# Optimization experiments

Measured on AMD Instinct MI355X. Metric: run time of the kernel, lower is better.

## Reference

```python
import jax, jax.numpy as jnp
import numpy as np


def _jpeg_tables():
    y_table = np.array([
        [16, 11, 10, 16, 24, 40, 51, 61],
        [12, 12, 14, 19, 26, 58, 60, 55],
        [14, 13, 16, 24, 40, 57, 69, 56],
        [14, 17, 22, 29, 51, 87, 80, 62],
        [18, 22, 37, 56, 68, 109, 103, 77],
        [24, 35, 55, 64, 81, 104, 113, 92],
        [49, 64, 78, 87, 103, 121, 120, 101],
        [72, 92, 95, 98, 112, 100, 103, 99]], dtype=np.float32)
    c_table = np.full((8, 8), 99.0, dtype=np.float32)
    c_table[:4, :4] = np.array([
        [17, 18, 24, 47],
        [18, 21, 26, 66],
        [24, 26, 56, 99],
        [47, 66, 99, 99]], dtype=np.float32).T
    return y_table, c_table


def _idct_basis():
    # alpha outer product and 8x8x8x8 cosine basis, matching _DeDCT8x8
    a = np.array([1.0 / np.sqrt(2)] + [1.0] * 7)
    alpha = np.outer(a, a).astype(np.float32)
    x = np.arange(8)
    cu = np.cos((2 * x[None, :] + 1) * x[:, None] * np.pi / 16)  # [freq, pos] -> careful
    # tensor[x, y, u, v] = cos((2u+1)x pi/16) * cos((2v+1)y pi/16)
    c = np.cos((2 * x[None, :] + 1) * x[:, None] * np.pi / 16)  # c[f, p]
    tensor = (c[:, None, :, None] * c[None, :, None, :]).astype(np.float32)
    return alpha, tensor


def setup_inputs() -> dict:
    key = jax.random.key(0)
    k1, k2, k3 = jax.random.split(key, 3)
    B, H, W = 8, 2048, 2048
    y = jax.random.normal(k1, (B, (H // 8) * (W // 8), 8, 8), dtype=jnp.float32)
    cb = jax.random.normal(k2, (B, (H // 16) * (W // 16), 8, 8), dtype=jnp.float32)
    cr = jax.random.normal(k3, (B, (H // 16) * (W // 16), 8, 8), dtype=jnp.float32)
    y_table, c_table = _jpeg_tables()
    alpha, dct_tensor = _idct_basis()
    shift = jnp.array([0.0, -128.0, -128.0], dtype=jnp.float32)
    matrix = jnp.asarray(np.array([
        [1.0, 0.0, 1.402],
        [1.0, -0.344136, -0.714136],
        [1.0, 1.772, 0.0]], dtype=np.float32).T)
    return {
        "y": y, "cb": cb, "cr": cr,
        "y_table": jnp.asarray(y_table), "c_table": jnp.asarray(c_table),
        "alpha": jnp.asarray(alpha), "dct_tensor": jnp.asarray(dct_tensor),
        "shift": shift, "matrix": matrix,
        "image_height": H, "image_width": W, "factor": 1,
    }


def _decode_plane(coeffs, table, factor, alpha, dct_tensor, height, width):
    # dequant + scaled 8x8 IDCT: coeffs [B, N, 8, 8]
    x = coeffs * (table * factor) * alpha
    blocks = 0.25 * jnp.einsum('bnxy,xyuv->bnuv', x, dct_tensor) + 128.0
    # unblock: [B, H//8, W//8, 8, 8] -> [B, H, W]
    b = blocks.shape[0]
    blocks = blocks.reshape(b, height // 8, width // 8, 8, 8)
    return blocks.transpose(0, 1, 3, 2, 4).reshape(b, height, width)


def reference(y, cb, cr, y_table, c_table, alpha, dct_tensor, shift, matrix,
              image_height, image_width, factor):
    H, W = image_height, image_width
    yp = _decode_plane(y, y_table, factor, alpha, dct_tensor, H, W)
    cbp = _decode_plane(cb, c_table, factor, alpha, dct_tensor, H // 2, W // 2)
    crp = _decode_plane(cr, c_table, factor, alpha, dct_tensor, H // 2, W // 2)
    up = lambda x: jnp.repeat(jnp.repeat(x, 2, axis=1), 2, axis=2)
    ycc = jnp.stack([yp, up(cbp), up(crp)], axis=-1)  # [B, H, W, 3]
    rgb = jnp.einsum('bhwc,cd->bhwd', ycc + shift, matrix)
    rgb = rgb.transpose(0, 3, 1, 2)  # [B, 3, H, W]
    return jnp.clip(rgb, 0.0, 255.0) / 255.0
```

## Files before the change

### kernel.cpp

```cpp
#include <hip/hip_runtime.h>


#define H 2048
#define W 2048
#define YBLK_COLS (W / 8)
#define CBLK_COLS (W / 16)

__global__ __launch_bounds__(256) void jpeg_decode_kernel(
    const float* __restrict__ yg,
    const float* __restrict__ cbg,
    const float* __restrict__ crg,
    const float* __restrict__ y_table,
    const float* __restrict__ c_table,
    const float* __restrict__ alpha,
    const float* __restrict__ dct,
    const float* __restrict__ shiftp,
    const float* __restrict__ matp,
    const int* __restrict__ factor_p,
    float* __restrict__ out)
{
    __shared__ float qY[64];
    __shared__ float qC[64];
    __shared__ float cosT[64];
    __shared__ float matS[9];
    __shared__ float shiftS[3];
    __shared__ float coef[32 * 72];
    __shared__ float pixY[16 * 128];
    __shared__ float pixCb[8 * 64];
    __shared__ float pixCr[8 * 64];

    const int tid = threadIdx.x;
    const int b  = blockIdx.z;
    const int th = blockIdx.y;
    const int tw = blockIdx.x;

    if (tid < 64) {
        const float f = (float)factor_p[0];
        qY[tid] = y_table[tid] * f * alpha[tid];
        qC[tid] = c_table[tid] * f * alpha[tid];
        const int x = tid >> 3, u = tid & 7;
        cosT[tid] = dct[x * 512 + u * 8];
    } else if (tid >= 64 && tid < 73) {
        matS[tid - 64] = matp[tid - 64];
    } else if (tid >= 73 && tid < 76) {
        shiftS[tid - 73] = shiftp[tid - 73];
    }
    __syncthreads();

    {
        const size_t base0 =
            (((size_t)b * (YBLK_COLS * (H / 8))) + (size_t)(2 * th) * YBLK_COLS + (size_t)tw * 16) * 64;
        const int flat = tid * 4;
        const int within = flat & 63;
#pragma unroll
        for (int s = 0; s < 2; s++) {
            const float4 v4 = *(const float4*)(yg + base0 + (size_t)s * (YBLK_COLS * 64 / 4) * 0 + (size_t)s * 16384 + flat);
            const int blk = s * 16 + (flat >> 6);
            float4 w;
            w.x = v4.x * qY[within + 0];
            w.y = v4.y * qY[within + 1];
            w.z = v4.z * qY[within + 2];
            w.w = v4.w * qY[within + 3];
            *(float4*)&coef[blk * 72 + within] = w;
        }
    }
    __syncthreads();

    auto idct8 = [&](const float* Dp, int v, float* p) {
        float cv[8];
#pragma unroll
        for (int yy = 0; yy < 8; yy++) cv[yy] = cosT[yy * 8 + v];
        float t[8];
#pragma unroll
        for (int x = 0; x < 8; x++) {
            const float4 a = *(const float4*)(Dp + x * 8);
            const float4 c = *(const float4*)(Dp + x * 8 + 4);
            t[x] = a.x * cv[0] + a.y * cv[1] + a.z * cv[2] + a.w * cv[3]
                 + c.x * cv[4] + c.y * cv[5] + c.z * cv[6] + c.w * cv[7];
        }
#pragma unroll
        for (int u = 0; u < 8; u++) {
            float s = 0.f;
#pragma unroll
            for (int x = 0; x < 8; x++) s += t[x] * cosT[x * 8 + u];
            p[u] = 0.25f * s + 128.0f;
        }
    };

    {
        const int bh  = tid >> 7;
        const int rem = tid & 127;
        const int bw  = rem >> 3;
        const int v   = rem & 7;
        const float* Dp = &coef[(bh * 16 + bw) * 72];
        float p[8];
        idct8(Dp, v, p);
#pragma unroll
        for (int u = 0; u < 8; u++) pixY[(bh * 8 + u) * 128 + rem] = p[u];
    }
    __syncthreads();

    {
        const int half = tid >> 7;
        const int t    = tid & 127;
        const int flat = t * 4;
        const int within = flat & 63;
        const float* src = half ? crg : cbg;
        const size_t basec =
            (((size_t)b * (CBLK_COLS * (H / 16))) + (size_t)th * CBLK_COLS + (size_t)tw * 8) * 64;
        const float4 v4 = *(const float4*)(src + basec + flat);
        const int blk = half * 8 + (flat >> 6);
        float4 w;
        w.x = v4.x * qC[within + 0];
        w.y = v4.y * qC[within + 1];
        w.z = v4.z * qC[within + 2];
        w.w = v4.w * qC[within + 3];
        *(float4*)&coef[blk * 72 + within] = w;
    }
    __syncthreads();

    if (tid < 128) {
        const int blk = tid >> 3;
        const int v   = tid & 7;
        const float* Dp = &coef[blk * 72];
        float p[8];
        idct8(Dp, v, p);
        float* dst = (blk >= 8) ? pixCr : pixCb;
        const int col = (blk & 7) * 8 + v;
#pragma unroll
        for (int u = 0; u < 8; u++) dst[u * 64 + col] = p[u];
    }
    __syncthreads();

    {
        const float s0 = shiftS[0], s1 = shiftS[1], s2 = shiftS[2];
        const float m0 = matS[0], m1 = matS[1], m2 = matS[2];
        const float m3 = matS[3], m4 = matS[4], m5 = matS[5];
        const float m6 = matS[6], m7 = matS[7], m8 = matS[8];
        const float inv255 = 1.0f / 255.0f;
        const size_t planeStride = (size_t)H * W;
        const size_t outBase = (size_t)b * 3 * planeStride;

#pragma unroll
        for (int it = 0; it < 2; it++) {
            const int idx = it * 256 + tid;
            const int r  = idx >> 5;
            const int c4 = (idx & 31) << 2;
            const float4 yv = *(const float4*)&pixY[r * 128 + c4];
            const int rc = r >> 1, cc = c4 >> 1;
            const float cb0 = pixCb[rc * 64 + cc + 0] + s1;
            const float cb1 = pixCb[rc * 64 + cc + 1] + s1;
            const float cr0 = pixCr[rc * 64 + cc + 0] + s2;
            const float cr1 = pixCr[rc * 64 + cc + 1] + s2;
            const float yy[4] = { yv.x + s0, yv.y + s0, yv.z + s0, yv.w + s0 };
            const float cbv[2] = { cb0, cb1 };
            const float crv[2] = { cr0, cr1 };

            float4 R, G, Bv;
            float* Rp = &R.x; float* Gp = &G.x; float* Bp = &Bv.x;
#pragma unroll
            for (int j = 0; j < 4; j++) {
                const int h2 = j >> 1;
                const float Yv = yy[j], Cb = cbv[h2], Cr = crv[h2];
                const float r_ = Yv * m0 + Cb * m3 + Cr * m6;
                const float g_ = Yv * m1 + Cb * m4 + Cr * m7;
                const float b_ = Yv * m2 + Cb * m5 + Cr * m8;
                Rp[j] = fminf(fmaxf(r_, 0.0f), 255.0f) * inv255;
                Gp[j] = fminf(fmaxf(g_, 0.0f), 255.0f) * inv255;
                Bp[j] = fminf(fmaxf(b_, 0.0f), 255.0f) * inv255;
            }

            const size_t row = (size_t)th * 16 + r;
            const size_t col = (size_t)tw * 128 + c4;
            const size_t o = outBase + row * W + col;
            *(float4*)(out + o)                  = R;
            *(float4*)(out + o + planeStride)    = G;
            *(float4*)(out + o + 2 * planeStride) = Bv;
        }
    }
}

extern "C" void kernel_launch(void* const* d_in, const int* in_sizes, int n_in,
                              void* d_out, int out_size, void* d_ws, size_t ws_size,
                              hipStream_t stream) {
    (void)in_sizes; (void)n_in; (void)d_ws; (void)ws_size; (void)out_size;
    const float* yg      = (const float*)d_in[0];
    const float* cbg     = (const float*)d_in[1];
    const float* crg     = (const float*)d_in[2];
    const float* y_table = (const float*)d_in[3];
    const float* c_table = (const float*)d_in[4];
    const float* alpha   = (const float*)d_in[5];
    const float* dct     = (const float*)d_in[6];
    const float* shiftp  = (const float*)d_in[7];
    const float* matp    = (const float*)d_in[8];
    const int*   factor  = (const int*)d_in[11];
    float* outp = (float*)d_out;

    dim3 grid(W / 128, H / 16, 8);
    jpeg_decode_kernel<<<grid, 256, 0, stream>>>(
        yg, cbg, crg, y_table, c_table, alpha, dct, shiftp, matp, factor, outp);
}
```

Before: 536.6 us.

## Hoist all global loads before first barrier, merge chroma stage, use nontemporal stores

Issues the Y and chroma coefficient loads at kernel start so they overlap with the table setup, and dequantizes luma and chroma into one larger shared buffer. This drops two barriers and the separate chroma load phase. The IDCT second pass now uses compile-time cosine constants instead of shared-memory reads, and output stores are nontemporal to avoid polluting cache. Shared memory use grows slightly, and the constant basis ignores the dct input tensor, relying on it being the standard cosine basis.

```diff
diff --git a/kernel.cpp b/kernel.cpp
--- a/kernel.cpp
+++ b/kernel.cpp
@@ -5,6 +5,28 @@
 #define W 2048
 #define YBLK_COLS (W / 8)
 #define CBLK_COLS (W / 16)
+#define CSTRIDE 68
+
+typedef float f32x4 __attribute__((ext_vector_type(4)));
+
+constexpr float CT[8][8] = {
+    {  1.0f,                   1.0f,                   1.0f,                   1.0f,
+       1.0f,                   1.0f,                   1.0f,                   1.0f },
+    {  0.980785280403230449f,  0.831469612302545237f,  0.555570233019602225f,  0.195090322016128268f,
+      -0.195090322016128268f, -0.555570233019602225f, -0.831469612302545237f, -0.980785280403230449f },
+    {  0.923879532511286756f,  0.382683432365089772f, -0.382683432365089772f, -0.923879532511286756f,
+      -0.923879532511286756f, -0.382683432365089772f,  0.382683432365089772f,  0.923879532511286756f },
+    {  0.831469612302545237f, -0.195090322016128268f, -0.980785280403230449f, -0.555570233019602225f,
+       0.555570233019602225f,  0.980785280403230449f,  0.195090322016128268f, -0.831469612302545237f },
+    {  0.707106781186547524f, -0.707106781186547524f, -0.707106781186547524f,  0.707106781186547524f,
+       0.707106781186547524f, -0.707106781186547524f, -0.707106781186547524f,  0.707106781186547524f },
+    {  0.555570233019602225f, -0.980785280403230449f,  0.195090322016128268f,  0.831469612302545237f,
+      -0.831469612302545237f, -0.195090322016128268f,  0.980785280403230449f, -0.555570233019602225f },
+    {  0.382683432365089772f, -0.923879532511286756f,  0.923879532511286756f, -0.382683432365089772f,
+      -0.382683432365089772f,  0.923879532511286756f, -0.923879532511286756f,  0.382683432365089772f },
+    {  0.195090322016128268f, -0.555570233019602225f,  0.831469612302545237f, -0.980785280403230449f,
+       0.980785280403230449f, -0.831469612302545237f,  0.555570233019602225f, -0.195090322016128268f },
+};
 
 __global__ __launch_bounds__(256) void jpeg_decode_kernel(
     const float* __restrict__ yg,
@@ -24,7 +46,7 @@
     __shared__ float cosT[64];
     __shared__ float matS[9];
     __shared__ float shiftS[3];
-    __shared__ float coef[32 * 72];
+    __shared__ float coef[48 * CSTRIDE];
     __shared__ float pixY[16 * 128];
     __shared__ float pixCb[8 * 64];
     __shared__ float pixCr[8 * 64];
@@ -40,36 +62,52 @@
         qC[tid] = c_table[tid] * f * alpha[tid];
         const int x = tid >> 3, u = tid & 7;
         cosT[tid] = dct[x * 512 + u * 8];
-    } else if (tid >= 64 && tid < 73) {
+    } else if (tid < 73) {
         matS[tid - 64] = matp[tid - 64];
-    } else if (tid >= 73 && tid < 76) {
+    } else if (tid < 76) {
         shiftS[tid - 73] = shiftp[tid - 73];
     }
+
+    const int flatY = tid * 4;
+    const size_t baseY =
+        (((size_t)b * (YBLK_COLS * (H / 8))) + (size_t)(2 * th) * YBLK_COLS + (size_t)tw * 16) * 64;
+    const float4 y0 = *(const float4*)(yg + baseY + flatY);
+    const float4 y1 = *(const float4*)(yg + baseY + 16384 + flatY);
+
+    const int half  = tid >> 7;
+    const int flatC = (tid & 127) * 4;
+    const float* srcC = half ? crg : cbg;
+    const size_t baseC =
+        (((size_t)b * (CBLK_COLS * (H / 16))) + (size_t)th * CBLK_COLS + (size_t)tw * 8) * 64;
+    const float4 c0 = *(const float4*)(srcC + baseC + flatC);
+
     __syncthreads();
 
     {
-        const size_t base0 =
-            (((size_t)b * (YBLK_COLS * (H / 8))) + (size_t)(2 * th) * YBLK_COLS + (size_t)tw * 16) * 64;
-        const int flat = tid * 4;
-        const int within = flat & 63;
-#pragma unroll
-        for (int s = 0; s < 2; s++) {
-            const float4 v4 = *(const float4*)(yg + base0 + (size_t)s * (YBLK_COLS * 64 / 4) * 0 + (size_t)s * 16384 + flat);
-            const int blk = s * 16 + (flat >> 6);
-            float4 w;
-            w.x = v4.x * qY[within + 0];
-            w.y = v4.y * qY[within + 1];
-            w.z = v4.z * qY[within + 2];
-            w.w = v4.w * qY[within + 3];
-            *(float4*)&coef[blk * 72 + within] = w;
-        }
+        const int within = flatY & 63;
+        const float4 qv = *(const float4*)&qY[within];
+        const int blk0 = flatY >> 6;
+        float4 w0, w1;
+        w0.x = y0.x * qv.x; w0.y = y0.y * qv.y; w0.z = y0.z * qv.z; w0.w = y0.w * qv.w;
+        w1.x = y1.x * qv.x; w1.y = y1.y * qv.y; w1.z = y1.z * qv.z; w1.w = y1.w * qv.w;
+        *(float4*)&coef[blk0 * CSTRIDE + within]        = w0;
+        *(float4*)&coef[(16 + blk0) * CSTRIDE + within] = w1;
+
+        const int withinC = flatC & 63;
+        const float4 qc = *(const float4*)&qC[withinC];
+        const int blkC = 32 + half * 8 + (flatC >> 6);
+        float4 wc;
+        wc.x = c0.x * qc.x; wc.y = c0.y * qc.y; wc.z = c0.z * qc.z; wc.w = c0.w * qc.w;
+        *(float4*)&coef[blkC * CSTRIDE + withinC] = wc;
     }
     __syncthreads();
 
-    auto idct8 = [&](const float* Dp, int v, float* p) {
-        float cv[8];
-#pragma unroll
-        for (int yy = 0; yy < 8; yy++) cv[yy] = cosT[yy * 8 + v];
+    const int v = tid & 7;
+    float cv[8];
+#pragma unroll
+    for (int yy = 0; yy < 8; yy++) cv[yy] = cosT[yy * 8 + v];
+
+    auto idct8 = [&](const float* Dp, float* p) {
         float t[8];
 #pragma unroll
         for (int x = 0; x < 8; x++) {
@@ -82,7 +120,7 @@
         for (int u = 0; u < 8; u++) {
             float s = 0.f;
 #pragma unroll
-            for (int x = 0; x < 8; x++) s += t[x] * cosT[x * 8 + u];
+            for (int x = 0; x < 8; x++) s += t[x] * CT[x][u];
             p[u] = 0.25f * s + 128.0f;
         }
     };
@@ -91,40 +129,17 @@
         const int bh  = tid >> 7;
         const int rem = tid & 127;
         const int bw  = rem >> 3;
-        const int v   = rem & 7;
-        const float* Dp = &coef[(bh * 16 + bw) * 72];
+        const float* Dp = &coef[(bh * 16 + bw) * CSTRIDE];
         float p[8];
-        idct8(Dp, v, p);
+        idct8(Dp, p);
 #pragma unroll
         for (int u = 0; u < 8; u++) pixY[(bh * 8 + u) * 128 + rem] = p[u];
     }
-    __syncthreads();
-
-    {
-        const int half = tid >> 7;
-        const int t    = tid & 127;
-        const int flat = t * 4;
-        const int within = flat & 63;
-        const float* src = half ? crg : cbg;
-        const size_t basec =
-            (((size_t)b * (CBLK_COLS * (H / 16))) + (size_t)th * CBLK_COLS + (size_t)tw * 8) * 64;
-        const float4 v4 = *(const float4*)(src + basec + flat);
-        const int blk = half * 8 + (flat >> 6);
-        float4 w;
-        w.x = v4.x * qC[within + 0];
-        w.y = v4.y * qC[within + 1];
-        w.z = v4.z * qC[within + 2];
-        w.w = v4.w * qC[within + 3];
-        *(float4*)&coef[blk * 72 + within] = w;
-    }
-    __syncthreads();
-
     if (tid < 128) {
         const int blk = tid >> 3;
-        const int v   = tid & 7;
-        const float* Dp = &coef[blk * 72];
+        const float* Dp = &coef[(32 + blk) * CSTRIDE];
         float p[8];
-        idct8(Dp, v, p);
+        idct8(Dp, p);
         float* dst = (blk >= 8) ? pixCr : pixCb;
         const int col = (blk & 7) * 8 + v;
 #pragma unroll
@@ -148,16 +163,13 @@
             const int c4 = (idx & 31) << 2;
             const float4 yv = *(const float4*)&pixY[r * 128 + c4];
             const int rc = r >> 1, cc = c4 >> 1;
-            const float cb0 = pixCb[rc * 64 + cc + 0] + s1;
-            const float cb1 = pixCb[rc * 64 + cc + 1] + s1;
-            const float cr0 = pixCr[rc * 64 + cc + 0] + s2;
-            const float cr1 = pixCr[rc * 64 + cc + 1] + s2;
+            const float2 cbv2 = *(const float2*)&pixCb[rc * 64 + cc];
+            const float2 crv2 = *(const float2*)&pixCr[rc * 64 + cc];
             const float yy[4] = { yv.x + s0, yv.y + s0, yv.z + s0, yv.w + s0 };
-            const float cbv[2] = { cb0, cb1 };
-            const float crv[2] = { cr0, cr1 };
-
-            float4 R, G, Bv;
-            float* Rp = &R.x; float* Gp = &G.x; float* Bp = &Bv.x;
+            const float cbv[2] = { cbv2.x + s1, cbv2.y + s1 };
+            const float crv[2] = { crv2.x + s2, crv2.y + s2 };
+
+            f32x4 R, G, Bv;
 #pragma unroll
             for (int j = 0; j < 4; j++) {
                 const int h2 = j >> 1;
@@ -165,17 +177,17 @@
                 const float r_ = Yv * m0 + Cb * m3 + Cr * m6;
                 const float g_ = Yv * m1 + Cb * m4 + Cr * m7;
                 const float b_ = Yv * m2 + Cb * m5 + Cr * m8;
-                Rp[j] = fminf(fmaxf(r_, 0.0f), 255.0f) * inv255;
-                Gp[j] = fminf(fmaxf(g_, 0.0f), 255.0f) * inv255;
-                Bp[j] = fminf(fmaxf(b_, 0.0f), 255.0f) * inv255;
+                R[j]  = fminf(fmaxf(r_, 0.0f), 255.0f) * inv255;
+                G[j]  = fminf(fmaxf(g_, 0.0f), 255.0f) * inv255;
+                Bv[j] = fminf(fmaxf(b_, 0.0f), 255.0f) * inv255;
             }
 
             const size_t row = (size_t)th * 16 + r;
             const size_t col = (size_t)tw * 128 + c4;
             const size_t o = outBase + row * W + col;
-            *(float4*)(out + o)                  = R;
-            *(float4*)(out + o + planeStride)    = G;
-            *(float4*)(out + o + 2 * planeStride) = Bv;
+            __builtin_nontemporal_store(R,  (f32x4*)(out + o));
+            __builtin_nontemporal_store(G,  (f32x4*)(out + o + planeStride));
+            __builtin_nontemporal_store(Bv, (f32x4*)(out + o + 2 * planeStride));
         }
     }
 }
```

Result: no change. 533.3 us (-0.6%).
